# Kernel tuning notes

Measured on AMD Instinct MI355X. Metric: run time of the kernel, lower is better.

The kernel has to match this reference:

```python
import jax, jax.numpy as jnp
import numpy as np

P = 399   # number of unshared per-position Conv1d kernels
K = 5     # conv kernel width (padding=2, 'same')


def _conv_stage(x, W, b):
    """Locally-connected stage: a distinct Conv1d per position along the last axis.
    x: [B, Cin, T, P]; W: [P, Cout, Cin, K]; b: [P, Cout] -> [B, Cout, T, P]."""
    xt = jnp.transpose(x, (3, 0, 1, 2))  # [P, B, Cin, T]

    def one(xi, wi, bi):
        y = jax.lax.conv_general_dilated(xi, wi, (1,), [(2, 2)],
                                         dimension_numbers=('NCH', 'OIH', 'NCH'))
        return y + bi[None, :, None]

    y = jax.vmap(one)(xt, W, b)          # [P, B, Cout, T]
    return jnp.transpose(y, (1, 2, 3, 0))


def _maxpool(x):
    # MaxPool2d((10,1), stride=(3,1)) over [B, C, T, P]
    return jax.lax.reduce_window(x, -jnp.inf, jax.lax.max,
                                 (1, 1, 10, 1), (1, 1, 3, 1), 'VALID')


def setup_inputs() -> dict:
    key = jax.random.key(0)
    ks = jax.random.split(key, 32)
    B, T = 256, 365

    def rn(k, shape, scale):
        return jax.random.normal(k, shape, jnp.float32) * scale

    d = {}
    d['x'] = jax.random.normal(ks[0], (B, T, P), jnp.float32)
    d['x2'] = jax.random.normal(ks[1], (B, 1307), jnp.float32)
    # per-position conv weights (PyTorch Conv1d layout O,I,K, stacked over P)
    d['W1'] = rn(ks[2], (P, 3, 1, K), 0.3); d['b1'] = rn(ks[3], (P, 3), 0.05)
    d['W2'] = rn(ks[4], (P, 3, 3, K), 0.2); d['b2'] = rn(ks[5], (P, 3), 0.05)
    d['W3'] = rn(ks[6], (P, 3, 3, K), 0.2); d['b3'] = rn(ks[7], (P, 3), 0.05)
    d['W4'] = rn(ks[8], (P, 3, 3, K), 0.2); d['b4'] = rn(ks[9], (P, 3), 0.05)
    # self.layers: 1307 -> 700 -> 200 -> 100
    d['lW1'] = rn(ks[10], (1307, 700), 0.02); d['lb1'] = rn(ks[11], (700,), 0.01)
    d['lW2'] = rn(ks[12], (700, 200), 0.03);  d['lb2'] = rn(ks[13], (200,), 0.01)
    d['lW3'] = rn(ks[14], (200, 100), 0.05);  d['lb3'] = rn(ks[15], (100,), 0.01)
    # self.common_layers: 1297 -> 500 -> 100 -> 20
    d['cW1'] = rn(ks[16], (1297, 500), 0.02); d['cb1'] = rn(ks[17], (500,), 0.01)
    d['cW2'] = rn(ks[18], (500, 100), 0.04);  d['cb2'] = rn(ks[19], (100,), 0.01)
    d['cW3'] = rn(ks[20], (100, 20), 0.08);   d['cb3'] = rn(ks[21], (20,), 0.01)
    # last_layer: 20 -> 1
    d['fW'] = rn(ks[22], (20, 1), 0.2);       d['fb'] = rn(ks[23], (1,), 0.01)
    return d


def reference(x, x2, W1, b1, W2, b2, W3, b3, W4, b4,
              lW1, lb1, lW2, lb2, lW3, lb3,
              cW1, cb1, cW2, cb2, cW3, cb3, fW, fb):
    h = x[:, None, :, :]                       # [B, 1, T, P]
    for W, b in ((W1, b1), (W2, b2), (W3, b3), (W4, b4)):
        h = _maxpool(jax.nn.relu(_conv_stage(h, W, b)))
    enc1 = h.reshape(h.shape[0], -1)           # [B, 3*1*399] = [B, 1197]

    e = jax.nn.relu(x2 @ lW1 + lb1)
    e = jax.nn.relu(e @ lW2 + lb2)
    enc2 = e @ lW3 + lb3                       # [B, 100] (no ReLU on final Linear)

    c = jnp.concatenate([enc1, enc2], axis=1)  # [B, 1297]
    c = jax.nn.relu(c @ cW1 + cb1)
    c = jax.nn.relu(c @ cW2 + cb2)
    c = jax.nn.relu(c @ cW3 + cb3)
    return c @ fW + fb                         # [B, 1]
```

## Files before the change

### kernel.cpp

```cpp
#include <hip/hip_runtime.h>

#define PP 399
#define BB 256


template<int SEG>
__device__ __forceinline__ float xload(const float* __restrict__ inp, int idx) {
    if (SEG == 2) {
        int ic = idx < 364 ? idx : 364;
        float v = inp[(long)ic * PP];
        return (idx <= 364) ? v : 0.f;
    }
    return inp[(long)idx * PP];
}

template<int OFF>
__device__ __forceinline__ void s1_group(const float (&xv)[13],
    const float (&w1)[3][5], const float (&B1)[3],
    float (&A1)[3], float (&c0)[3])
{
#pragma unroll
    for (int co = 0; co < 3; ++co) {
        float a0 = B1[co], a1 = B1[co], a2 = B1[co];
#pragma unroll
        for (int t = 0; t < 5; ++t) {
            a0 = fmaf(xv[OFF + t],     w1[co][t], a0);
            a1 = fmaf(xv[OFF + 1 + t], w1[co][t], a1);
            a2 = fmaf(xv[OFF + 2 + t], w1[co][t], a2);
        }
        c0[co] = a0;
        A1[co] = fmaxf(fmaxf(a0, a1), a2);
    }
}

template<int P2>
__device__ __forceinline__ void s2_step(
    float (&fe)[3][4], const float (&e)[3],
    const float (&w2)[3][3][5], const float (&B2)[3],
    float (&A2a)[3], float (&A2b)[3], float (&A2c)[3], float (&A2cur)[3],
    float*& op, bool do_c2, bool do_emit)
{
    if (do_c2) {
        float c2v[3];
#pragma unroll
        for (int co = 0; co < 3; ++co) {
            float a = B2[co];
#pragma unroll
            for (int ci = 0; ci < 3; ++ci) {
                a = fmaf(fe[ci][0], w2[co][ci][0], a);
                a = fmaf(fe[ci][1], w2[co][ci][1], a);
                a = fmaf(fe[ci][2], w2[co][ci][2], a);
                a = fmaf(fe[ci][3], w2[co][ci][3], a);
                a = fmaf(e[ci],     w2[co][ci][4], a);
            }
            c2v[co] = a;
        }
        if (P2 == 0) {
#pragma unroll
            for (int co = 0; co < 3; ++co) { A2a[co] = A2b[co]; A2b[co] = A2c[co]; A2c[co] = A2cur[co]; }
            if (do_emit) {
#pragma unroll
                for (int co = 0; co < 3; ++co)
                    op[co * PP] = fmaxf(fmaxf(fmaxf(fmaxf(A2a[co], A2b[co]), A2c[co]), c2v[co]), 0.f);
                op += 3 * PP;
            }
#pragma unroll
            for (int co = 0; co < 3; ++co) A2cur[co] = c2v[co];
        } else {
#pragma unroll
            for (int co = 0; co < 3; ++co) A2cur[co] = fmaxf(A2cur[co], c2v[co]);
        }
    }
#pragma unroll
    for (int ci = 0; ci < 3; ++ci) {
        fe[ci][0] = fe[ci][1]; fe[ci][1] = fe[ci][2]; fe[ci][2] = fe[ci][3]; fe[ci][3] = e[ci];
    }
}

template<int P2>
__device__ __forceinline__ void emit_e(
    const float (&Aa)[3], const float (&Ab)[3], const float (&Ac)[3],
    const float (&c0)[3],
    float (&fe)[3][4],
    const float (&w2)[3][3][5], const float (&B2)[3],
    float (&A2a)[3], float (&A2b)[3], float (&A2c)[3], float (&A2cur)[3],
    float*& op, bool do_c2, bool do_emit)
{
    float e[3];
#pragma unroll
    for (int co = 0; co < 3; ++co)
        e[co] = fmaxf(fmaxf(fmaxf(fmaxf(Aa[co], Ab[co]), Ac[co]), c0[co]), 0.f);
    s2_step<P2>(fe, e, w2, B2, A2a, A2b, A2c, A2cur, op, do_c2, do_emit);
}

template<int SEG>
__device__ __forceinline__ void s12_body(
    const float* __restrict__ x,
    const float* __restrict__ W1, const float* __restrict__ b1,
    const float* __restrict__ W2, const float* __restrict__ b2,
    float* __restrict__ h2, int b, int p)
{
    constexpr int J0tab[4] = {0, 13, 25, 37};
    constexpr int j0 = J0tab[SEG];
    constexpr int j1 = J0tab[SEG + 1];
    constexpr int k0 = (SEG == 0) ? 0 : 3 * j0 - 2;
    constexpr int kend = (3 * j1 + 11 < 121) ? (3 * j1 + 11) : 121;
    constexpr int NGRP = kend - k0 + 1;
    constexpr int NS = NGRP / 3;
    constexpr int NREM = NGRP - 3 * NS;
    constexpr int c2start = (SEG == 0) ? 5 : (k0 + 7);
    constexpr int e2start = 3 * j0 + 14;
    constexpr int P2_0 = (SEG == 0) ? 1 : 2;
    constexpr int P2_1 = (SEG == 0) ? 2 : 0;
    constexpr int P2_2 = (SEG == 0) ? 0 : 1;

    float w1[3][5], B1[3];
    {
        const float* wp = W1 + (long)p * 15;
#pragma unroll
        for (int co = 0; co < 3; ++co) {
#pragma unroll
            for (int t = 0; t < 5; ++t) w1[co][t] = wp[co * 5 + t];
            B1[co] = b1[(long)p * 3 + co];
        }
    }
    float w2[3][3][5], B2[3];
    {
        const float* wp = W2 + (long)p * 45;
#pragma unroll
        for (int co = 0; co < 3; ++co) {
#pragma unroll
            for (int ci = 0; ci < 3; ++ci)
#pragma unroll
                for (int t = 0; t < 5; ++t) w2[co][ci][t] = wp[(co * 3 + ci) * 5 + t];
            B2[co] = b2[(long)p * 3 + co];
        }
    }

    const float* __restrict__ inp = x + (long)b * 365 * PP + p;
    float* op = h2 + ((long)b * 37 + j0) * 3 * PP + p;

    float xv[13];
#pragma unroll
    for (int s = 0; s < 13; ++s) {
        int idx = 3 * k0 - 2 + s;
        xv[s] = (idx >= 0) ? inp[(long)idx * PP] : 0.f;
    }
    float q1[9];
#pragma unroll
    for (int s = 0; s < 9; ++s)
        q1[s] = xload<SEG>(inp, 3 * k0 + 11 + s);

    float fe[3][4];
    float A1p[3][3];
    float A2a[3], A2b[3], A2c[3], A2cur[3];
#pragma unroll
    for (int ci = 0; ci < 3; ++ci)
#pragma unroll
        for (int s = 0; s < 4; ++s) fe[ci][s] = 0.f;
#pragma unroll
    for (int co = 0; co < 3; ++co) {
        A1p[0][co] = 0.f; A1p[1][co] = 0.f; A1p[2][co] = 0.f;
        A2a[co] = 0.f; A2b[co] = 0.f; A2c[co] = 0.f; A2cur[co] = 0.f;
    }

    for (int S = 0; S < NS; ++S) {
        int k = k0 + 3 * S;
        float q2[9];
#pragma unroll
        for (int s = 0; s < 9; ++s)
            q2[s] = xload<SEG>(inp, 3 * k + 20 + s);

        float A1c0[3], A1c1[3], A1c2[3], c0[3];

        s1_group<0>(xv, w1, B1, A1c0, c0);
        if (S >= 1)
            emit_e<P2_0>(A1p[0], A1p[1], A1p[2], c0, fe, w2, B2,
                         A2a, A2b, A2c, A2cur, op,
                         k >= c2start, k >= e2start);
        s1_group<3>(xv, w1, B1, A1c1, c0);
        if (S >= 1)
            emit_e<P2_1>(A1p[1], A1p[2], A1c0, c0, fe, w2, B2,
                         A2a, A2b, A2c, A2cur, op,
                         k + 1 >= c2start, k + 1 >= e2start);
        s1_group<6>(xv, w1, B1, A1c2, c0);
        if (S >= 1)
            emit_e<P2_2>(A1p[2], A1c0, A1c1, c0, fe, w2, B2,
                         A2a, A2b, A2c, A2cur, op,
                         k + 2 >= c2start, k + 2 >= e2start);

#pragma unroll
        for (int co = 0; co < 3; ++co) {
            A1p[0][co] = A1c0[co]; A1p[1][co] = A1c1[co]; A1p[2][co] = A1c2[co];
        }
        xv[0] = xv[9]; xv[1] = xv[10]; xv[2] = xv[11]; xv[3] = xv[12];
#pragma unroll
        for (int s = 0; s < 9; ++s) { xv[4 + s] = q1[s]; q1[s] = q2[s]; }
    }

    if constexpr (NREM >= 1) {
        int k = k0 + 3 * NS;
        float A1c0[3], c0[3];
        s1_group<0>(xv, w1, B1, A1c0, c0);
        emit_e<P2_0>(A1p[0], A1p[1], A1p[2], c0, fe, w2, B2,
                     A2a, A2b, A2c, A2cur, op,
                     k >= c2start, k >= e2start);
        if constexpr (NREM >= 2) {
            float A1c1[3];
            s1_group<3>(xv, w1, B1, A1c1, c0);
            emit_e<P2_1>(A1p[1], A1p[2], A1c0, c0, fe, w2, B2,
                         A2a, A2b, A2c, A2cur, op,
                         k + 1 >= c2start, k + 1 >= e2start);
        }
    }
    if constexpr (SEG == 2) {
        float ez[3] = {0.f, 0.f, 0.f};
        s2_step<0>(fe, ez, w2, B2, A2a, A2b, A2c, A2cur, op, true, true);
    }
}

__global__ __launch_bounds__(64)
void conv_s12(const float* __restrict__ x,
              const float* __restrict__ W1, const float* __restrict__ b1,
              const float* __restrict__ W2, const float* __restrict__ b2,
              float* __restrict__ h2)
{
    int gid = blockIdx.x * 64 + threadIdx.x;
    if (gid >= BB * PP) return;
    int b = gid / PP;
    int p = gid - b * PP;
    if (blockIdx.y == 0)      s12_body<0>(x, W1, b1, W2, b2, h2, b, p);
    else if (blockIdx.y == 1) s12_body<1>(x, W1, b1, W2, b2, h2, b, p);
    else                      s12_body<2>(x, W1, b1, W2, b2, h2, b, p);
}

template<int CIN>
struct Stage {
    float w[3][CIN][5];
    float b[3];
    float xw[CIN][5];
    float m1[3], m2[3], m3[3];
    int nin;
};

__device__ __forceinline__ void init_s3(Stage<3>& s, const float* __restrict__ Wt,
                                        const float* __restrict__ Bs, int p) {
    const float* wp = Wt + (long)p * 45;
#pragma unroll
    for (int co = 0; co < 3; ++co)
#pragma unroll
        for (int ci = 0; ci < 3; ++ci)
#pragma unroll
            for (int k = 0; k < 5; ++k)
                s.w[co][ci][k] = wp[(co * 3 + ci) * 5 + k];
#pragma unroll
    for (int co = 0; co < 3; ++co) s.b[co] = Bs[(long)p * 3 + co];
#pragma unroll
    for (int ci = 0; ci < 3; ++ci)
#pragma unroll
        for (int k = 0; k < 5; ++k) s.xw[ci][k] = 0.f;
#pragma unroll
    for (int co = 0; co < 3; ++co) { s.m1[co] = -1e30f; s.m2[co] = -1e30f; s.m3[co] = -1e30f; }
    s.nin = 0;
}

template<int CIN>
__device__ __forceinline__ bool feed(Stage<CIN>& s, const float* in, float* out) {
#pragma unroll
    for (int ci = 0; ci < CIN; ++ci) {
        s.xw[ci][0] = s.xw[ci][1];
        s.xw[ci][1] = s.xw[ci][2];
        s.xw[ci][2] = s.xw[ci][3];
        s.xw[ci][3] = s.xw[ci][4];
        s.xw[ci][4] = in[ci];
    }
    int t = s.nin - 2;
    s.nin++;
    if (t < 0) return false;

    float c[3];
#pragma unroll
    for (int co = 0; co < 3; ++co) {
        float a = s.b[co];
#pragma unroll
        for (int ci = 0; ci < CIN; ++ci)
#pragma unroll
            for (int k = 0; k < 5; ++k)
                a = fmaf(s.xw[ci][k], s.w[co][ci][k], a);
        c[co] = fmaxf(a, 0.f);
    }

    bool emit = false;
    int ph = t % 3;
    if (ph == 0) {
        if (t >= 9) {
#pragma unroll
            for (int co = 0; co < 3; ++co) out[co] = fmaxf(s.m1[co], c[co]);
            emit = true;
        }
#pragma unroll
        for (int co = 0; co < 3; ++co) {
            float a = fmaxf(s.m2[co], c[co]);
            float bb = fmaxf(s.m3[co], c[co]);
            s.m1[co] = a; s.m2[co] = bb; s.m3[co] = c[co];
        }
    } else {
#pragma unroll
        for (int co = 0; co < 3; ++co) {
            s.m1[co] = fmaxf(s.m1[co], c[co]);
            s.m2[co] = fmaxf(s.m2[co], c[co]);
            s.m3[co] = fmaxf(s.m3[co], c[co]);
        }
    }
    return emit;
}

__global__ __launch_bounds__(64)
void conv_s34(const float* __restrict__ h2,
              const float* __restrict__ W3, const float* __restrict__ b3,
              const float* __restrict__ W4, const float* __restrict__ b4,
              float* __restrict__ cbuf)
{
    int gid = blockIdx.x * 64 + threadIdx.x;
    if (gid >= BB * PP) return;
    int b = gid / PP;
    int p = gid - b * PP;

    Stage<3> s3, s4;
    init_s3(s3, W3, b3, p);
    init_s3(s4, W4, b4, p);

    const float* inp = h2 + (long)b * 37 * 3 * PP + p;
    float* o4 = cbuf + (long)b * 1297 + p;

    float v3[3], v4[3];
    float z[3] = {0.f, 0.f, 0.f};

    float r0[3], r1[3], r2[3], r3[3], r4[3];
#pragma unroll
    for (int ci = 0; ci < 3; ++ci) {
        r0[ci] = inp[(long)(0 * 3 + ci) * PP];
        r1[ci] = inp[(long)(1 * 3 + ci) * PP];
        r2[ci] = inp[(long)(2 * 3 + ci) * PP];
        r3[ci] = inp[(long)(3 * 3 + ci) * PP];
        r4[ci] = inp[(long)(4 * 3 + ci) * PP];
    }

    for (int i = 0; i < 39; ++i) {
        float nn[3];
        int i5 = i + 5;
#pragma unroll
        for (int ci = 0; ci < 3; ++ci)
            nn[ci] = (i5 < 37) ? inp[(long)(i5 * 3 + ci) * PP] : 0.f;
        if (feed(s3, r0, v3)) {
            if (feed(s4, v3, v4)) {
#pragma unroll
                for (int co = 0; co < 3; ++co) o4[co * PP] = v4[co];
            }
        }
#pragma unroll
        for (int ci = 0; ci < 3; ++ci) {
            r0[ci] = r1[ci]; r1[ci] = r2[ci]; r2[ci] = r3[ci]; r3[ci] = r4[ci]; r4[ci] = nn[ci];
        }
    }
    for (int r = 0; r < 2; ++r) {
        if (feed(s4, z, v4)) {
#pragma unroll
            for (int co = 0; co < 3; ++co) o4[co * PP] = v4[co];
        }
    }
}

template<int RELU_A>
__global__ __launch_bounds__(256)
void gemm_atomic(const float* __restrict__ A,
                 const float* __restrict__ Wt,
                 float* __restrict__ out,
                 int K, int N, int lda, int ldo, int kchunk)
{
    __shared__ float As[32][36];
    __shared__ float Bs[32][36];

    int tid = threadIdx.x;
    int ty  = tid >> 3;
    int tx4 = (tid & 7) * 4;
    int c0 = blockIdx.x * 32;
    int m0 = blockIdx.y * 32;
    int k0 = blockIdx.z * kchunk;
    int klim = min(K, k0 + kchunk);

    float4 acc = make_float4(0.f, 0.f, 0.f, 0.f);

    for (int kb = k0; kb < klim; kb += 32) {
#pragma unroll
        for (int j = 0; j < 4; ++j) {
            int kk = kb + tx4 + j;
            float v = (kk < klim) ? A[(long)(m0 + ty) * lda + kk] : 0.f;
            if (RELU_A) v = fmaxf(v, 0.f);
            As[ty][tx4 + j] = v;
        }
#pragma unroll
        for (int j = 0; j < 4; ++j) {
            int kk = kb + ty;
            int c = c0 + tx4 + j;
            Bs[ty][tx4 + j] = (kk < klim && c < N) ? Wt[(long)kk * N + c] : 0.f;
        }
        __syncthreads();
#pragma unroll
        for (int kk = 0; kk < 32; ++kk) {
            float a = As[ty][kk];
            float4 bv = *(const float4*)&Bs[kk][tx4];
            acc.x = fmaf(a, bv.x, acc.x);
            acc.y = fmaf(a, bv.y, acc.y);
            acc.z = fmaf(a, bv.z, acc.z);
            acc.w = fmaf(a, bv.w, acc.w);
        }
        __syncthreads();
    }

    long m = m0 + ty;
    if (c0 + tx4 + 0 < N) atomicAdd(&out[m * ldo + c0 + tx4 + 0], acc.x);
    if (c0 + tx4 + 1 < N) atomicAdd(&out[m * ldo + c0 + tx4 + 1], acc.y);
    if (c0 + tx4 + 2 < N) atomicAdd(&out[m * ldo + c0 + tx4 + 2], acc.z);
    if (c0 + tx4 + 3 < N) atomicAdd(&out[m * ldo + c0 + tx4 + 3], acc.w);
}

__global__ __launch_bounds__(256)
void init_bias(float* __restrict__ e1, const float* __restrict__ lb1,
               float* __restrict__ e2, const float* __restrict__ lb2,
               float* __restrict__ enc2, const float* __restrict__ lb3,
               float* __restrict__ c1, const float* __restrict__ cb1,
               float* __restrict__ c2, const float* __restrict__ cb2,
               float* __restrict__ c3, const float* __restrict__ cb3)
{
    int idx = blockIdx.x * 256 + threadIdx.x;
    if (idx < BB * 700) { e1[idx] = lb1[idx % 700]; return; }
    idx -= BB * 700;
    if (idx < BB * 200) { e2[idx] = lb2[idx % 200]; return; }
    idx -= BB * 200;
    if (idx < BB * 100) { int m = idx / 100, c = idx % 100; enc2[(long)m * 1297 + c] = lb3[c]; return; }
    idx -= BB * 100;
    if (idx < BB * 500) { c1[idx] = cb1[idx % 500]; return; }
    idx -= BB * 500;
    if (idx < BB * 100) { c2[idx] = cb2[idx % 100]; return; }
    idx -= BB * 100;
    if (idx < BB * 20)  { c3[idx] = cb3[idx % 20]; return; }
}

__global__ __launch_bounds__(64)
void final_kernel(const float* __restrict__ c3,
                  const float* __restrict__ fW,
                  const float* __restrict__ fb,
                  float* __restrict__ out)
{
    int m = blockIdx.x * 64 + threadIdx.x;
    if (m >= BB) return;
    float acc = fb[0];
#pragma unroll
    for (int k = 0; k < 20; ++k)
        acc = fmaf(fmaxf(c3[m * 20 + k], 0.f), fW[k], acc);
    out[m] = acc;
}

extern "C" void kernel_launch(void* const* d_in, const int* in_sizes, int n_in,
                              void* d_out, int out_size, void* d_ws, size_t ws_size,
                              hipStream_t stream)
{
    const float* x   = (const float*)d_in[0];
    const float* x2  = (const float*)d_in[1];
    const float* W1  = (const float*)d_in[2];
    const float* b1  = (const float*)d_in[3];
    const float* W2  = (const float*)d_in[4];
    const float* b2  = (const float*)d_in[5];
    const float* W3  = (const float*)d_in[6];
    const float* b3  = (const float*)d_in[7];
    const float* W4  = (const float*)d_in[8];
    const float* b4  = (const float*)d_in[9];
    const float* lW1 = (const float*)d_in[10];
    const float* lb1 = (const float*)d_in[11];
    const float* lW2 = (const float*)d_in[12];
    const float* lb2 = (const float*)d_in[13];
    const float* lW3 = (const float*)d_in[14];
    const float* lb3 = (const float*)d_in[15];
    const float* cW1 = (const float*)d_in[16];
    const float* cb1 = (const float*)d_in[17];
    const float* cW2 = (const float*)d_in[18];
    const float* cb2 = (const float*)d_in[19];
    const float* cW3 = (const float*)d_in[20];
    const float* cb3 = (const float*)d_in[21];
    const float* fW  = (const float*)d_in[22];
    const float* fb  = (const float*)d_in[23];
    float* out = (float*)d_out;

    float* ws = (float*)d_ws;
    const long n_h2   = (long)BB * 37 * 3 * PP;
    const long n_cbuf = (long)BB * 1297;
    float* h2   = ws;
    float* cbuf = h2 + n_h2;
    float* e1   = cbuf + n_cbuf;
    float* e2   = e1 + (long)BB * 700;
    float* c1   = e2 + (long)BB * 200;
    float* c2   = c1 + (long)BB * 500;
    float* c3b  = c2 + (long)BB * 100;

    init_bias<<<1620, 256, 0, stream>>>(e1, lb1, e2, lb2, cbuf + 1197, lb3,
                                        c1, cb1, c2, cb2, c3b, cb3);

    conv_s12<<<dim3(1596, 3), 64, 0, stream>>>(x, W1, b1, W2, b2, h2);
    conv_s34<<<1596, 64, 0, stream>>>(h2, W3, b3, W4, b4, cbuf);

    gemm_atomic<0><<<dim3(22, 8, 6), 256, 0, stream>>>(x2, lW1, e1, 1307, 700, 1307, 700, 256);
    gemm_atomic<1><<<dim3( 7, 8, 6), 256, 0, stream>>>(e1, lW2, e2,  700, 200,  700, 200, 128);
    gemm_atomic<1><<<dim3( 4, 8, 4), 256, 0, stream>>>(e2, lW3, cbuf + 1197, 200, 100, 200, 1297, 64);

    gemm_atomic<0><<<dim3(16, 8, 6), 256, 0, stream>>>(cbuf, cW1, c1, 1297, 500, 1297, 500, 256);
    gemm_atomic<1><<<dim3( 4, 8, 8), 256, 0, stream>>>(c1, cW2, c2, 500, 100, 500, 100, 64);
    gemm_atomic<1><<<dim3( 1, 8, 4), 256, 0, stream>>>(c2, cW3, c3b, 100, 20, 100, 20, 32);

    final_kernel<<<dim3(4), 64, 0, stream>>>(c3b, fW, fb, out);
}
```

Baseline: 199.6 us.

## Co-launch conv stages with independent MLP GEMMs via merged block ranges

```diff
diff --git a/kernel.cpp b/kernel.cpp
--- a/kernel.cpp
+++ b/kernel.cpp
@@ -146,10 +146,6 @@
         int idx = 3 * k0 - 2 + s;
         xv[s] = (idx >= 0) ? inp[(long)idx * PP] : 0.f;
     }
-    float q1[9];
-#pragma unroll
-    for (int s = 0; s < 9; ++s)
-        q1[s] = xload<SEG>(inp, 3 * k0 + 11 + s);
 
     float fe[3][4];
     float A1p[3][3];
@@ -166,10 +162,10 @@
 
     for (int S = 0; S < NS; ++S) {
         int k = k0 + 3 * S;
-        float q2[9];
+        float q[9];
 #pragma unroll
         for (int s = 0; s < 9; ++s)
-            q2[s] = xload<SEG>(inp, 3 * k + 20 + s);
+            q[s] = xload<SEG>(inp, 3 * k + 11 + s);
 
         float A1c0[3], A1c1[3], A1c2[3], c0[3];
 
@@ -195,7 +191,7 @@
         }
         xv[0] = xv[9]; xv[1] = xv[10]; xv[2] = xv[11]; xv[3] = xv[12];
 #pragma unroll
-        for (int s = 0; s < 9; ++s) { xv[4 + s] = q1[s]; q1[s] = q2[s]; }
+        for (int s = 0; s < 9; ++s) xv[4 + s] = q[s];
     }
 
     if constexpr (NREM >= 1) {
@@ -219,19 +215,93 @@
     }
 }
 
-__global__ __launch_bounds__(64)
-void conv_s12(const float* __restrict__ x,
-              const float* __restrict__ W1, const float* __restrict__ b1,
-              const float* __restrict__ W2, const float* __restrict__ b2,
-              float* __restrict__ h2)
-{
-    int gid = blockIdx.x * 64 + threadIdx.x;
-    if (gid >= BB * PP) return;
-    int b = gid / PP;
-    int p = gid - b * PP;
-    if (blockIdx.y == 0)      s12_body<0>(x, W1, b1, W2, b2, h2, b, p);
-    else if (blockIdx.y == 1) s12_body<1>(x, W1, b1, W2, b2, h2, b, p);
-    else                      s12_body<2>(x, W1, b1, W2, b2, h2, b, p);
+template<int RELU_A>
+__device__ __forceinline__ void gemm_tile(
+    const float* __restrict__ A, const float* __restrict__ Wt,
+    float* __restrict__ out, int K, int N, int lda, int ldo, int kchunk,
+    int bx, int by, int bz)
+{
+    __shared__ float As[32][36];
+    __shared__ float Bs[32][36];
+
+    int tid = threadIdx.x;
+    int ty  = tid >> 3;
+    int tx4 = (tid & 7) * 4;
+    int c0 = bx * 32;
+    int m0 = by * 32;
+    int k0 = bz * kchunk;
+    int klim = min(K, k0 + kchunk);
+
+    float4 acc = make_float4(0.f, 0.f, 0.f, 0.f);
+
+    for (int kb = k0; kb < klim; kb += 32) {
+#pragma unroll
+        for (int j = 0; j < 4; ++j) {
+            int kk = kb + tx4 + j;
+            float v = (kk < klim) ? A[(long)(m0 + ty) * lda + kk] : 0.f;
+            if (RELU_A) v = fmaxf(v, 0.f);
+            As[ty][tx4 + j] = v;
+        }
+#pragma unroll
+        for (int j = 0; j < 4; ++j) {
+            int kk = kb + ty;
+            int c = c0 + tx4 + j;
+            Bs[ty][tx4 + j] = (kk < klim && c < N) ? Wt[(long)kk * N + c] : 0.f;
+        }
+        __syncthreads();
+#pragma unroll
+        for (int kk = 0; kk < 32; ++kk) {
+            float a = As[ty][kk];
+            float4 bv = *(const float4*)&Bs[kk][tx4];
+            acc.x = fmaf(a, bv.x, acc.x);
+            acc.y = fmaf(a, bv.y, acc.y);
+            acc.z = fmaf(a, bv.z, acc.z);
+            acc.w = fmaf(a, bv.w, acc.w);
+        }
+        __syncthreads();
+    }
+
+    long m = m0 + ty;
+    if (c0 + tx4 + 0 < N) atomicAdd(&out[m * ldo + c0 + tx4 + 0], acc.x);
+    if (c0 + tx4 + 1 < N) atomicAdd(&out[m * ldo + c0 + tx4 + 1], acc.y);
+    if (c0 + tx4 + 2 < N) atomicAdd(&out[m * ldo + c0 + tx4 + 2], acc.z);
+    if (c0 + tx4 + 3 < N) atomicAdd(&out[m * ldo + c0 + tx4 + 3], acc.w);
+}
+
+template<int RELU_A>
+__global__ __launch_bounds__(256)
+void gemm_atomic(const float* __restrict__ A, const float* __restrict__ Wt,
+                 float* __restrict__ out, int K, int N, int lda, int ldo, int kchunk)
+{
+    gemm_tile<RELU_A>(A, Wt, out, K, N, lda, ldo, kchunk,
+                      blockIdx.x, blockIdx.y, blockIdx.z);
+}
+
+__global__ __launch_bounds__(256)
+void d1_conv_s12_lw1(const float* __restrict__ x,
+                     const float* __restrict__ W1, const float* __restrict__ b1,
+                     const float* __restrict__ W2, const float* __restrict__ b2,
+                     float* __restrict__ h2,
+                     const float* __restrict__ x2, const float* __restrict__ lW1,
+                     float* __restrict__ e1)
+{
+    int blk = blockIdx.x;
+    if (blk < 1197) {
+        int seg = blk / 399;
+        int bx  = blk - seg * 399;
+        int gid = bx * 256 + threadIdx.x;
+        int b = gid / PP;
+        int p = gid - b * PP;
+        if (seg == 0)      s12_body<0>(x, W1, b1, W2, b2, h2, b, p);
+        else if (seg == 1) s12_body<1>(x, W1, b1, W2, b2, h2, b, p);
+        else               s12_body<2>(x, W1, b1, W2, b2, h2, b, p);
+    } else {
+        int g = blk - 1197;
+        int gx = g % 22;
+        int gy = (g / 22) % 8;
+        int gz = g / 176;
+        gemm_tile<0>(x2, lW1, e1, 1307, 700, 1307, 700, 256, gx, gy, gz);
+    }
 }
 
 template<int CIN>
@@ -315,17 +385,12 @@
     return emit;
 }
 
-__global__ __launch_bounds__(64)
-void conv_s34(const float* __restrict__ h2,
-              const float* __restrict__ W3, const float* __restrict__ b3,
-              const float* __restrict__ W4, const float* __restrict__ b4,
-              float* __restrict__ cbuf)
-{
-    int gid = blockIdx.x * 64 + threadIdx.x;
-    if (gid >= BB * PP) return;
-    int b = gid / PP;
-    int p = gid - b * PP;
-
+__device__ __forceinline__ void s34_body(
+    const float* __restrict__ h2,
+    const float* __restrict__ W3, const float* __restrict__ b3,
+    const float* __restrict__ W4, const float* __restrict__ b4,
+    float* __restrict__ cbuf, int b, int p)
+{
     Stage<3> s3, s4;
     init_s3(s3, W3, b3, p);
     init_s3(s4, W4, b4, p);
@@ -371,58 +436,27 @@
     }
 }
 
-template<int RELU_A>
 __global__ __launch_bounds__(256)
-void gemm_atomic(const float* __restrict__ A,
-                 const float* __restrict__ Wt,
-                 float* __restrict__ out,
-                 int K, int N, int lda, int ldo, int kchunk)
-{
-    __shared__ float As[32][36];
-    __shared__ float Bs[32][36];
-
-    int tid = threadIdx.x;
-    int ty  = tid >> 3;
-    int tx4 = (tid & 7) * 4;
-    int c0 = blockIdx.x * 32;
-    int m0 = blockIdx.y * 32;
-    int k0 = blockIdx.z * kchunk;
-    int klim = min(K, k0 + kchunk);
-
-    float4 acc = make_float4(0.f, 0.f, 0.f, 0.f);
-
-    for (int kb = k0; kb < klim; kb += 32) {
-#pragma unroll
-        for (int j = 0; j < 4; ++j) {
-            int kk = kb + tx4 + j;
-            float v = (kk < klim) ? A[(long)(m0 + ty) * lda + kk] : 0.f;
-            if (RELU_A) v = fmaxf(v, 0.f);
-            As[ty][tx4 + j] = v;
-        }
-#pragma unroll
-        for (int j = 0; j < 4; ++j) {
-            int kk = kb + ty;
-            int c = c0 + tx4 + j;
-            Bs[ty][tx4 + j] = (kk < klim && c < N) ? Wt[(long)kk * N + c] : 0.f;
-        }
-        __syncthreads();
-#pragma unroll
-        for (int kk = 0; kk < 32; ++kk) {
-            float a = As[ty][kk];
-            float4 bv = *(const float4*)&Bs[kk][tx4];
-            acc.x = fmaf(a, bv.x, acc.x);
-            acc.y = fmaf(a, bv.y, acc.y);
-            acc.z = fmaf(a, bv.z, acc.z);
-            acc.w = fmaf(a, bv.w, acc.w);
-        }
-        __syncthreads();
-    }
-
-    long m = m0 + ty;
-    if (c0 + tx4 + 0 < N) atomicAdd(&out[m * ldo + c0 + tx4 + 0], acc.x);
-    if (c0 + tx4 + 1 < N) atomicAdd(&out[m * ldo + c0 + tx4 + 1], acc.y);
-    if (c0 + tx4 + 2 < N) atomicAdd(&out[m * ldo + c0 + tx4 + 2], acc.z);
-    if (c0 + tx4 + 3 < N) atomicAdd(&out[m * ldo + c0 + tx4 + 3], acc.w);
+void d2_conv_s34_lw2(const float* __restrict__ h2,
+                     const float* __restrict__ W3, const float* __restrict__ b3,
+                     const float* __restrict__ W4, const float* __restrict__ b4,
+                     float* __restrict__ cbuf,
+                     const float* __restrict__ e1, const float* __restrict__ lW2,
+                     float* __restrict__ e2)
+{
+    int blk = blockIdx.x;
+    if (blk < 399) {
+        int gid = blk * 256 + threadIdx.x;
+        int b = gid / PP;
+        int p = gid - b * PP;
+        s34_body(h2, W3, b3, W4, b4, cbuf, b, p);
+    } else {
+        int g = blk - 399;
+        int gx = g % 7;
+        int gy = (g / 7) % 8;
+        int gz = g / 56;
+        gemm_tile<1>(e1, lW2, e2, 700, 200, 700, 200, 128, gx, gy, gz);
+    }
 }
 
 __global__ __launch_bounds__(256)
@@ -506,12 +540,11 @@
     init_bias<<<1620, 256, 0, stream>>>(e1, lb1, e2, lb2, cbuf + 1197, lb3,
                                         c1, cb1, c2, cb2, c3b, cb3);
 
-    conv_s12<<<dim3(1596, 3), 64, 0, stream>>>(x, W1, b1, W2, b2, h2);
-    conv_s34<<<1596, 64, 0, stream>>>(h2, W3, b3, W4, b4, cbuf);
-
-    gemm_atomic<0><<<dim3(22, 8, 6), 256, 0, stream>>>(x2, lW1, e1, 1307, 700, 1307, 700, 256);
-    gemm_atomic<1><<<dim3( 7, 8, 6), 256, 0, stream>>>(e1, lW2, e2,  700, 200,  700, 200, 128);
-    gemm_atomic<1><<<dim3( 4, 8, 4), 256, 0, stream>>>(e2, lW3, cbuf + 1197, 200, 100, 200, 1297, 64);
+    d1_conv_s12_lw1<<<1197 + 1056, 256, 0, stream>>>(x, W1, b1, W2, b2, h2,
+                                                     x2, lW1, e1);
+    d2_conv_s34_lw2<<<399 + 336, 256, 0, stream>>>(h2, W3, b3, W4, b4, cbuf,
+                                                   e1, lW2, e2);
+    gemm_atomic<1><<<dim3(4, 8, 4), 256, 0, stream>>>(e2, lW3, cbuf + 1197, 200, 100, 200, 1297, 64);
 
     gemm_atomic<0><<<dim3(16, 8, 6), 256, 0, stream>>>(cbuf, cW1, c1, 1297, 500, 1297, 500, 256);
     gemm_atomic<1><<<dim3( 4, 8, 8), 256, 0, stream>>>(c1, cW2, c2, 500, 100, 500, 100, 64);
```

Result: faster. 161.6 us (-19.1%).
